# Performance work log

Hardware: AMD Instinct MI355X
Metric: run time of the kernel (lower is better)

The kernel has to match this reference:

```python
import jax, jax.numpy as jnp
import numpy as np

B, C, H, W = 256, 1024, 7, 7
D_HID, N_CLS = 768, 5

def setup_inputs() -> dict:
    key = jax.random.key(0)
    k1, k2, k3, k4, k5 = jax.random.split(key, 5)
    flat = C * H * W  # 50176
    return {
        "features": jax.random.normal(k1, (B, C, H, W), dtype=jnp.float32),
        "W1": jax.random.normal(k2, (D_HID, flat), dtype=jnp.float32) * 0.02,
        "b1": jax.random.normal(k3, (D_HID,), dtype=jnp.float32) * 0.02,
        "W2": jax.random.normal(k4, (N_CLS, D_HID), dtype=jnp.float32) * 0.02,
        "b2": jax.random.normal(k5, (N_CLS,), dtype=jnp.float32) * 0.02,
    }

def reference(features, W1, b1, W2, b2):
    # PCAM: per-(batch, channel) global max over spatial dims, broadcast-multiplied
    # back onto the feature map. Replaces the torch Python double loop with one
    # fused reduce-max + elementwise multiply.
    ch_max = jnp.max(features, axis=(2, 3), keepdims=True)  # [B, C, 1, 1]
    pcams = features * ch_max                               # [B, C, H, W]
    flat = pcams.reshape(pcams.shape[0], -1)                # [B, C*H*W]
    h = jax.nn.relu(flat @ W1.T + b1)                       # [B, 768]
    logits = h @ W2.T + b2                                  # [B, num_classes]
    return (logits, features)
```

## Files before the change

kernel.cpp:

```cpp
#include <hip/hip_runtime.h>
#include <hip/hip_bf16.h>

#define B_SZ   256
#define C_SZ   1024
#define HW     49
#define KDIM   50176
#define DHID   768
#define NCLS   5

typedef __bf16 bf16x8 __attribute__((ext_vector_type(8)));
typedef __bf16 bf16x4 __attribute__((ext_vector_type(4)));
typedef float  f32x4  __attribute__((ext_vector_type(4)));

#define GLOAD_LDS16(gsrc, ldst) \
  __builtin_amdgcn_global_load_lds((__attribute__((address_space(1))) void*)(gsrc), \
                                   (__attribute__((address_space(3))) void*)(ldst), 16, 0, 0)

#define BARRIER() do { \
    asm volatile("s_waitcnt lgkmcnt(0)" ::: "memory"); \
    __builtin_amdgcn_s_barrier(); \
    asm volatile("" ::: "memory"); \
  } while (0)

__global__ __launch_bounds__(256) void pcam_kernel(const float* __restrict__ feat,
                                                   float* __restrict__ feat_out,
                                                   __bf16* __restrict__ pcam) {
  __shared__ float sv[1568];
  __shared__ float smax[32];
  const int tid = threadIdx.x;
  const size_t base = (size_t)blockIdx.x * 1568;

  const float4* src4 = (const float4*)(feat + base);
  float4* dst4 = (float4*)(feat_out + base);
  #pragma unroll
  for (int i = 0; i < 2; ++i) {
    int idx = tid + i * 256;
    if (idx < 392) {
      float4 v = src4[idx];
      dst4[idx] = v;
      ((float4*)sv)[idx] = v;
    }
  }
  __syncthreads();

  {
    const int r = tid >> 3, p = tid & 7;
    float mx = -INFINITY;
    for (int i = p; i < HW; i += 8) mx = fmaxf(mx, sv[r * HW + i]);
    #pragma unroll
    for (int off = 1; off < 8; off <<= 1) mx = fmaxf(mx, __shfl_xor(mx, off));
    if (p == 0) smax[r] = mx;
  }
  __syncthreads();

  for (int i = tid; i < 1568; i += 256) {
    int r = (i * 1338) >> 16;
    float v = sv[i] * smax[r];
    pcam[base + i] = (__bf16)v;
  }
}

#define BM 256
#define BN 128
#define BK 64
#define NT 6
#define KSPLIT 42
#define KSTEPS 784

__global__ __launch_bounds__(512, 1) void gemm1_kernel(const __bf16* __restrict__ pcam,
                                                       const float* __restrict__ W1,
                                                       __bf16* __restrict__ h_part) {
  __shared__ __bf16 Asm[2][BM * BK];
  __shared__ __bf16 Bsm[2][BN * BK];

  const int tid  = threadIdx.x;
  const int lane = tid & 63;
  const int w    = tid >> 6;
  const int c_   = lane & 15;
  const int q_   = lane >> 4;
  const int n0   = blockIdx.x * BN;
  const int ks   = blockIdx.y;
  const int s0   = (ks * KSTEPS) / KSPLIT;
  const int s1   = ((ks + 1) * KSTEPS) / KSPLIT;

  unsigned a_off[4];
  #pragma unroll
  for (int it = 0; it < 4; ++it) {
    const unsigned ug = it * 512 + tid;
    const unsigned m  = ug >> 3;
    a_off[it] = m * (unsigned)KDIM + (((ug & 7) ^ (m & 7)) * 8u);
  }

  const float* bsrc[4];
  #pragma unroll
  for (int i = 0; i < 4; ++i)
    bsrc[i] = W1 + (size_t)(n0 + w * 16 + i * 4 + q_) * KDIM + c_ * 4;

  int bwr[4];
  #pragma unroll
  for (int i = 0; i < 4; ++i) {
    const int r = w * 16 + i * 4 + q_;
    bwr[i] = r * 128 + (((c_ >> 1) ^ (r & 7)) << 4) + ((c_ & 1) << 3);
  }
  const int rn = w * 16 + c_;

  f32x4 acc[16];
  #pragma unroll
  for (int i = 0; i < 16; ++i) acc[i] = f32x4{0.f, 0.f, 0.f, 0.f};

  f32x4 bq0, bq1, bq2, bq3;

#define ISSUE_A(bi, s) do { \
    const unsigned ka = (unsigned)(s) * BK; \
    _Pragma("unroll") \
    for (int it = 0; it < 4; ++it) \
      GLOAD_LDS16(pcam + a_off[it] + ka, (char*)Asm[bi] + it * 8192 + w * 1024); \
  } while (0)

#define ISSUE_B(s) do { \
    const size_t kb = (size_t)(s) * BK; \
    bq0 = *(const f32x4*)(bsrc[0] + kb); \
    bq1 = *(const f32x4*)(bsrc[1] + kb); \
    bq2 = *(const f32x4*)(bsrc[2] + kb); \
    bq3 = *(const f32x4*)(bsrc[3] + kb); \
  } while (0)

#define WRITE_B(bi) do { \
    _Pragma("unroll") \
    for (int i = 0; i < 4; ++i) { \
      const f32x4 v = (i == 0) ? bq0 : (i == 1) ? bq1 : (i == 2) ? bq2 : bq3; \
      bf16x4 bv; \
      bv[0] = (__bf16)v[0]; bv[1] = (__bf16)v[1]; \
      bv[2] = (__bf16)v[2]; bv[3] = (__bf16)v[3]; \
      *(bf16x4*)((char*)Bsm[bi] + bwr[i]) = bv; \
    } \
  } while (0)

#define COMPUTE(bi) do { \
    _Pragma("unroll") \
    for (int ksub = 0; ksub < 2; ++ksub) { \
      const int u = ksub * 4 + q_; \
      const bf16x8 bfr = *(const bf16x8*)((const char*)Bsm[bi] + rn * 128 + ((u ^ (rn & 7)) << 4)); \
      _Pragma("unroll") \
      for (int i = 0; i < 16; ++i) { \
        const int m = i * 16 + c_; \
        const bf16x8 af = *(const bf16x8*)((const char*)Asm[bi] + m * 128 + ((u ^ (m & 7)) << 4)); \
        acc[i] = __builtin_amdgcn_mfma_f32_16x16x32_bf16(af, bfr, acc[i], 0, 0, 0); \
      } \
    } \
  } while (0)

  ISSUE_A(0, s0);
  ISSUE_B(s0);
  asm volatile("s_waitcnt vmcnt(0)" ::: "memory");
  WRITE_B(0);
  BARRIER();
  if (s0 + 1 < s1) { ISSUE_A(1, s0 + 1); ISSUE_B(s0 + 1); }

  for (int s = s0; s < s1; ++s) {
    const int cur = (s - s0) & 1;
    COMPUTE(cur);
    if (s + 1 < s1) {
      asm volatile("s_waitcnt vmcnt(0)" ::: "memory");
      WRITE_B(cur ^ 1);
    }
    BARRIER();
    if (s + 2 < s1) { ISSUE_A(cur, s + 2); ISSUE_B(s + 2); }
  }

  __bf16* out = h_part + (size_t)ks * DHID * B_SZ;
  const int n = n0 + w * 16 + c_;
  #pragma unroll
  for (int i = 0; i < 16; ++i) {
    const int mb = i * 16 + q_ * 4;
    bf16x4 pv;
    pv[0] = (__bf16)acc[i][0]; pv[1] = (__bf16)acc[i][1];
    pv[2] = (__bf16)acc[i][2]; pv[3] = (__bf16)acc[i][3];
    *(bf16x4*)(out + (size_t)n * B_SZ + mb) = pv;
  }
#undef ISSUE_A
#undef ISSUE_B
#undef WRITE_B
#undef COMPUTE
}

__global__ __launch_bounds__(256) void reduce_kernel(const __bf16* __restrict__ h_part,
                                                     const float* __restrict__ b1,
                                                     float* __restrict__ h) {
  const int n = blockIdx.x;
  const int m = threadIdx.x;
  float s = 0.f;
  #pragma unroll 6
  for (int ks = 0; ks < KSPLIT; ++ks)
    s += (float)h_part[((size_t)ks * DHID + n) * B_SZ + m];
  float v = s + b1[n];
  h[(size_t)m * DHID + n] = v > 0.f ? v : 0.f;
}

__global__ __launch_bounds__(64) void head_kernel(const float* __restrict__ h,
                                                  const float* __restrict__ W2,
                                                  const float* __restrict__ b2,
                                                  float* __restrict__ logits) {
  const int m = blockIdx.x;
  const int lane = threadIdx.x;
  float hv[12];
  #pragma unroll
  for (int j = 0; j < 12; ++j) hv[j] = h[(size_t)m * DHID + j * 64 + lane];
  #pragma unroll
  for (int c = 0; c < NCLS; ++c) {
    float s = 0.f;
    #pragma unroll
    for (int j = 0; j < 12; ++j) s += hv[j] * W2[c * DHID + j * 64 + lane];
    #pragma unroll
    for (int off = 32; off > 0; off >>= 1) s += __shfl_xor(s, off);
    if (lane == 0) logits[m * NCLS + c] = s + b2[c];
  }
}

extern "C" void kernel_launch(void* const* d_in, const int* in_sizes, int n_in,
                              void* d_out, int out_size, void* d_ws, size_t ws_size,
                              hipStream_t stream) {
  const float* feat = (const float*)d_in[0];
  const float* W1   = (const float*)d_in[1];
  const float* b1   = (const float*)d_in[2];
  const float* W2   = (const float*)d_in[3];
  const float* b2   = (const float*)d_in[4];

  float* logits   = (float*)d_out;
  float* feat_out = (float*)d_out + (size_t)B_SZ * NCLS;

  char* ws = (char*)d_ws;
  __bf16* pcam   = (__bf16*)ws;
  __bf16* h_part = (__bf16*)(ws + (size_t)B_SZ * KDIM * 2);
  float*  h      = (float*)(ws + (size_t)B_SZ * KDIM * 2
                               + (size_t)KSPLIT * DHID * B_SZ * 2);

  pcam_kernel<<<(B_SZ * C_SZ) / 32, 256, 0, stream>>>(feat, feat_out, pcam);
  gemm1_kernel<<<dim3(NT, KSPLIT), 512, 0, stream>>>(pcam, W1, h_part);
  reduce_kernel<<<DHID, 256, 0, stream>>>(h_part, b1, h);
  head_kernel<<<B_SZ, 64, 0, stream>>>(h, W2, b2, logits);
}
```

Before: 93.93 us.

## Widen GEMM N-tile to 256, rebalance split-K, and double-buffer W1 register prefetch

The GEMM block tile grows from 128 to 256 output columns, so each A fragment read from shared memory feeds two MFMAs. The grid changes from 6x42 to 3x85 so the total block count stays about the same. W1 loads now use two register sets and are issued two steps ahead, with partial vmcnt waits instead of full drains, so global latency overlaps compute. This doubles the accumulator registers and raises the split-K partial count, which increases the work in the reduce kernel.

```diff
diff --git a/kernel.cpp b/kernel.cpp
--- a/kernel.cpp
+++ b/kernel.cpp
@@ -16,6 +16,7 @@
   __builtin_amdgcn_global_load_lds((__attribute__((address_space(1))) void*)(gsrc), \
                                    (__attribute__((address_space(3))) void*)(ldst), 16, 0, 0)
 
+#define FENCE()   asm volatile("" ::: "memory")
 #define BARRIER() do { \
     asm volatile("s_waitcnt lgkmcnt(0)" ::: "memory"); \
     __builtin_amdgcn_s_barrier(); \
@@ -61,10 +62,10 @@
 }
 
 #define BM 256
-#define BN 128
+#define BN 256
 #define BK 64
-#define NT 6
-#define KSPLIT 42
+#define NT 3
+#define KSPLIT 85
 #define KSTEPS 784
 
 __global__ __launch_bounds__(512, 1) void gemm1_kernel(const __bf16* __restrict__ pcam,
@@ -91,44 +92,48 @@
     a_off[it] = m * (unsigned)KDIM + (((ug & 7) ^ (m & 7)) * 8u);
   }
 
-  const float* bsrc[4];
-  #pragma unroll
-  for (int i = 0; i < 4; ++i)
-    bsrc[i] = W1 + (size_t)(n0 + w * 16 + i * 4 + q_) * KDIM + c_ * 4;
-
-  int bwr[4];
-  #pragma unroll
-  for (int i = 0; i < 4; ++i) {
-    const int r = w * 16 + i * 4 + q_;
+  const float* bbase = W1 + (size_t)(n0 + w * 32 + q_) * KDIM + c_ * 4;
+  int bwr[8];
+  #pragma unroll
+  for (int i = 0; i < 8; ++i) {
+    const int r = w * 32 + i * 4 + q_;
     bwr[i] = r * 128 + (((c_ >> 1) ^ (r & 7)) << 4) + ((c_ & 1) << 3);
   }
-  const int rn = w * 16 + c_;
-
-  f32x4 acc[16];
-  #pragma unroll
-  for (int i = 0; i < 16; ++i) acc[i] = f32x4{0.f, 0.f, 0.f, 0.f};
-
-  f32x4 bq0, bq1, bq2, bq3;
+
+  f32x4 acc[16][2];
+  #pragma unroll
+  for (int i = 0; i < 16; ++i)
+    #pragma unroll
+    for (int j = 0; j < 2; ++j) acc[i][j] = f32x4{0.f, 0.f, 0.f, 0.f};
+
+  f32x4 pA0, pA1, pA2, pA3, pA4, pA5, pA6, pA7;
+  f32x4 pB0, pB1, pB2, pB3, pB4, pB5, pB6, pB7;
+
+#define ISSUE_B8(Q0,Q1,Q2,Q3,Q4,Q5,Q6,Q7, s) do { \
+    const size_t kb = (size_t)(s) * BK; \
+    Q0 = *(const f32x4*)(bbase + kb + (size_t)( 0) * KDIM); \
+    Q1 = *(const f32x4*)(bbase + kb + (size_t)( 4) * KDIM); \
+    Q2 = *(const f32x4*)(bbase + kb + (size_t)( 8) * KDIM); \
+    Q3 = *(const f32x4*)(bbase + kb + (size_t)(12) * KDIM); \
+    Q4 = *(const f32x4*)(bbase + kb + (size_t)(16) * KDIM); \
+    Q5 = *(const f32x4*)(bbase + kb + (size_t)(20) * KDIM); \
+    Q6 = *(const f32x4*)(bbase + kb + (size_t)(24) * KDIM); \
+    Q7 = *(const f32x4*)(bbase + kb + (size_t)(28) * KDIM); \
+    FENCE(); \
+  } while (0)
 
 #define ISSUE_A(bi, s) do { \
     const unsigned ka = (unsigned)(s) * BK; \
     _Pragma("unroll") \
     for (int it = 0; it < 4; ++it) \
       GLOAD_LDS16(pcam + a_off[it] + ka, (char*)Asm[bi] + it * 8192 + w * 1024); \
-  } while (0)
-
-#define ISSUE_B(s) do { \
-    const size_t kb = (size_t)(s) * BK; \
-    bq0 = *(const f32x4*)(bsrc[0] + kb); \
-    bq1 = *(const f32x4*)(bsrc[1] + kb); \
-    bq2 = *(const f32x4*)(bsrc[2] + kb); \
-    bq3 = *(const f32x4*)(bsrc[3] + kb); \
-  } while (0)
-
-#define WRITE_B(bi) do { \
+    FENCE(); \
+  } while (0)
+
+#define WRITE_B8(bi, Q0,Q1,Q2,Q3,Q4,Q5,Q6,Q7) do { \
     _Pragma("unroll") \
-    for (int i = 0; i < 4; ++i) { \
-      const f32x4 v = (i == 0) ? bq0 : (i == 1) ? bq1 : (i == 2) ? bq2 : bq3; \
+    for (int i = 0; i < 8; ++i) { \
+      const f32x4 v = (i==0)?Q0:(i==1)?Q1:(i==2)?Q2:(i==3)?Q3:(i==4)?Q4:(i==5)?Q5:(i==6)?Q6:Q7; \
       bf16x4 bv; \
       bv[0] = (__bf16)v[0]; bv[1] = (__bf16)v[1]; \
       bv[2] = (__bf16)v[2]; bv[3] = (__bf16)v[3]; \
@@ -140,47 +145,67 @@
     _Pragma("unroll") \
     for (int ksub = 0; ksub < 2; ++ksub) { \
       const int u = ksub * 4 + q_; \
-      const bf16x8 bfr = *(const bf16x8*)((const char*)Bsm[bi] + rn * 128 + ((u ^ (rn & 7)) << 4)); \
+      bf16x8 bfr[2]; \
+      _Pragma("unroll") \
+      for (int j = 0; j < 2; ++j) { \
+        const int rn = w * 32 + j * 16 + c_; \
+        bfr[j] = *(const bf16x8*)((const char*)Bsm[bi] + rn * 128 + ((u ^ (rn & 7)) << 4)); \
+      } \
       _Pragma("unroll") \
       for (int i = 0; i < 16; ++i) { \
         const int m = i * 16 + c_; \
         const bf16x8 af = *(const bf16x8*)((const char*)Asm[bi] + m * 128 + ((u ^ (m & 7)) << 4)); \
-        acc[i] = __builtin_amdgcn_mfma_f32_16x16x32_bf16(af, bfr, acc[i], 0, 0, 0); \
+        acc[i][0] = __builtin_amdgcn_mfma_f32_16x16x32_bf16(af, bfr[0], acc[i][0], 0, 0, 0); \
+        acc[i][1] = __builtin_amdgcn_mfma_f32_16x16x32_bf16(af, bfr[1], acc[i][1], 0, 0, 0); \
       } \
     } \
   } while (0)
 
+  ISSUE_B8(pA0,pA1,pA2,pA3,pA4,pA5,pA6,pA7, s0);
   ISSUE_A(0, s0);
-  ISSUE_B(s0);
-  asm volatile("s_waitcnt vmcnt(0)" ::: "memory");
-  WRITE_B(0);
+  if (s0 + 1 < s1) {
+    ISSUE_B8(pB0,pB1,pB2,pB3,pB4,pB5,pB6,pB7, s0 + 1);
+    asm volatile("s_waitcnt vmcnt(8)" ::: "memory");
+  } else {
+    asm volatile("s_waitcnt vmcnt(0)" ::: "memory");
+  }
+  WRITE_B8(0, pA0,pA1,pA2,pA3,pA4,pA5,pA6,pA7);
   BARRIER();
-  if (s0 + 1 < s1) { ISSUE_A(1, s0 + 1); ISSUE_B(s0 + 1); }
+  if (s0 + 1 < s1) ISSUE_A(1, s0 + 1);
 
   for (int s = s0; s < s1; ++s) {
     const int cur = (s - s0) & 1;
+    if (s + 2 < s1) {
+      if (cur == 0) ISSUE_B8(pA0,pA1,pA2,pA3,pA4,pA5,pA6,pA7, s + 2);
+      else          ISSUE_B8(pB0,pB1,pB2,pB3,pB4,pB5,pB6,pB7, s + 2);
+    }
     COMPUTE(cur);
     if (s + 1 < s1) {
-      asm volatile("s_waitcnt vmcnt(0)" ::: "memory");
-      WRITE_B(cur ^ 1);
-    }
-    BARRIER();
-    if (s + 2 < s1) { ISSUE_A(cur, s + 2); ISSUE_B(s + 2); }
+      if (s + 2 < s1) asm volatile("s_waitcnt vmcnt(8)" ::: "memory");
+      else            asm volatile("s_waitcnt vmcnt(0)" ::: "memory");
+      if (cur == 0) WRITE_B8(1, pB0,pB1,pB2,pB3,pB4,pB5,pB6,pB7);
+      else          WRITE_B8(0, pA0,pA1,pA2,pA3,pA4,pA5,pA6,pA7);
+      BARRIER();
+      if (s + 2 < s1) ISSUE_A(cur, s + 2);
+    }
   }
 
   __bf16* out = h_part + (size_t)ks * DHID * B_SZ;
-  const int n = n0 + w * 16 + c_;
-  #pragma unroll
-  for (int i = 0; i < 16; ++i) {
-    const int mb = i * 16 + q_ * 4;
-    bf16x4 pv;
-    pv[0] = (__bf16)acc[i][0]; pv[1] = (__bf16)acc[i][1];
-    pv[2] = (__bf16)acc[i][2]; pv[3] = (__bf16)acc[i][3];
-    *(bf16x4*)(out + (size_t)n * B_SZ + mb) = pv;
-  }
+  #pragma unroll
+  for (int j = 0; j < 2; ++j) {
+    const int n = n0 + w * 32 + j * 16 + c_;
+    #pragma unroll
+    for (int i = 0; i < 16; ++i) {
+      const int mb = i * 16 + q_ * 4;
+      bf16x4 pv;
+      pv[0] = (__bf16)acc[i][j][0]; pv[1] = (__bf16)acc[i][j][1];
+      pv[2] = (__bf16)acc[i][j][2]; pv[3] = (__bf16)acc[i][j][3];
+      *(bf16x4*)(out + (size_t)n * B_SZ + mb) = pv;
+    }
+  }
+#undef ISSUE_B8
 #undef ISSUE_A
-#undef ISSUE_B
-#undef WRITE_B
+#undef WRITE_B8
 #undef COMPUTE
 }
 
@@ -190,7 +215,7 @@
   const int n = blockIdx.x;
   const int m = threadIdx.x;
   float s = 0.f;
-  #pragma unroll 6
+  #pragma unroll 5
   for (int ks = 0; ks < KSPLIT; ++ks)
     s += (float)h_part[((size_t)ks * DHID + n) * B_SZ + m];
   float v = s + b1[n];
```

Measured after the change: 95.97 us. 1.02x slower.
